# Performance work log

Hardware: AMD Instinct MI355X
Metric: run time of the kernel (lower is better)

The kernel has to match this reference:

```python
import jax, jax.numpy as jnp
import numpy as np
import math

D_MODEL = 1024
HEADS = 16
D_K = D_MODEL // HEADS
BATCH = 4
SEQ = 1024


def setup_inputs() -> dict:
    key = jax.random.key(0)
    ks = jax.random.split(key, 12)
    s = 1.0 / math.sqrt(D_MODEL)
    inp = {
        "q": jax.random.normal(ks[0], (BATCH, SEQ, D_MODEL), jnp.float32),
        "k": jax.random.normal(ks[1], (BATCH, SEQ, D_MODEL), jnp.float32),
        "v": jax.random.normal(ks[2], (BATCH, SEQ, D_MODEL), jnp.float32),
        # causal mask, broadcastable over (batch, heads)
        "mask": jnp.tril(jnp.ones((SEQ, SEQ), jnp.bool_))[None, None, :, :],
        "Wq": jax.random.normal(ks[3], (D_MODEL, D_MODEL), jnp.float32) * s,
        "bq": jax.random.normal(ks[4], (D_MODEL,), jnp.float32) * 0.01,
        "Wk": jax.random.normal(ks[5], (D_MODEL, D_MODEL), jnp.float32) * s,
        "bk": jax.random.normal(ks[6], (D_MODEL,), jnp.float32) * 0.01,
        "Wv": jax.random.normal(ks[7], (D_MODEL, D_MODEL), jnp.float32) * s,
        "bv": jax.random.normal(ks[8], (D_MODEL,), jnp.float32) * 0.01,
        "Wo": jax.random.normal(ks[9], (D_MODEL, D_MODEL), jnp.float32) * s,
        "bo": jax.random.normal(ks[10], (D_MODEL,), jnp.float32) * 0.01,
    }
    return inp


def reference(q, k, v, mask, Wq, bq, Wk, bk, Wv, bv, Wo, bo):
    B, S, _ = q.shape
    # projections (torch Linear: x @ W.T + b; here W stored as [in, out])
    def proj(x, W, b):
        return (x @ W + b).reshape(B, -1, HEADS, D_K).transpose(0, 2, 1, 3)

    Q = proj(q, Wq, bq)  # [B, H, S, Dk]
    K = proj(k, Wk, bk)
    V = proj(v, Wv, bv)

    scores = jnp.einsum("bhqd,bhkd->bhqk", Q, K) / math.sqrt(D_K)
    scores = jnp.where(mask, scores, jnp.float32(-1e9))
    attn = jax.nn.softmax(scores, axis=-1)  # dropout p=0.0 -> identity
    x = jnp.einsum("bhqk,bhkd->bhqd", attn, V)
    x = x.transpose(0, 2, 1, 3).reshape(B, S, D_MODEL)
    return x @ Wo + bo
```

## Files before the change

kernel.cpp:

```cpp
#include <hip/hip_runtime.h>
#include <math.h>

typedef __bf16 bf16_t;
typedef bf16_t bf16x8 __attribute__((ext_vector_type(8)));
typedef bf16_t bf16x4 __attribute__((ext_vector_type(4)));
typedef float  floatx4 __attribute__((ext_vector_type(4)));
typedef unsigned int u32;

#define MFMA_BF16(a, b, c) __builtin_amdgcn_mfma_f32_16x16x32_bf16((a), (b), (c), 0, 0, 0)

#if __has_builtin(__builtin_amdgcn_exp2f)
#define EXP2F(x) __builtin_amdgcn_exp2f(x)
#else
#define EXP2F(x) exp2f(x)
#endif

static constexpr int DMODEL = 1024;
static constexpr int NHEAD  = 16;
static constexpr int HDIM   = 64;
static constexpr int NBATCH = 4;
static constexpr int SEQLEN = 1024;
static constexpr int NTOK   = NBATCH * SEQLEN;

typedef __attribute__((address_space(3))) void       as3_void;
typedef __attribute__((address_space(1))) const void as1_cvoid;

__device__ __forceinline__ void gload16(const void* g, void* l) {
    __builtin_amdgcn_global_load_lds((as1_cvoid*)g, (as3_void*)l, 16, 0, 0);
}

__device__ __forceinline__ bf16x8 load_cvt8(const float* __restrict__ p) {
    floatx4 a = *(const floatx4*)p;
    floatx4 b = *(const floatx4*)(p + 4);
    bf16x8 r;
    r[0] = (bf16_t)a[0]; r[1] = (bf16_t)a[1]; r[2] = (bf16_t)a[2]; r[3] = (bf16_t)a[3];
    r[4] = (bf16_t)b[0]; r[5] = (bf16_t)b[1]; r[6] = (bf16_t)b[2]; r[7] = (bf16_t)b[3];
    return r;
}

__global__ __launch_bounds__(256) void prep(
    const float* __restrict__ W0, const float* __restrict__ W1,
    const float* __restrict__ W2, const float* __restrict__ W3,
    const float* __restrict__ q, const float* __restrict__ k, const float* __restrict__ v,
    bf16_t* __restrict__ Wt, bf16_t* __restrict__ Xr)
{
    __shared__ float tile[32][33];
    const int z = blockIdx.z;
    if (z < 4) {
        const float* W = (z == 0) ? W0 : (z == 1) ? W1 : (z == 2) ? W2 : W3;
        bf16_t* O = Wt + (size_t)z * DMODEL * DMODEL;
        const int tx = threadIdx.x & 31, ty = threadIdx.x >> 5;
        const int r0 = blockIdx.x * 32, c0 = blockIdx.y * 32;
#pragma unroll
        for (int i = 0; i < 32; i += 8)
            tile[ty + i][tx] = W[(size_t)(r0 + ty + i) * DMODEL + c0 + tx];
        __syncthreads();
#pragma unroll
        for (int i = 0; i < 32; i += 8)
            O[(size_t)(c0 + ty + i) * DMODEL + r0 + tx] = (bf16_t)tile[tx][ty + i];
    } else {
        const float* src = (z == 4) ? q : (z == 5) ? k : v;
        bf16_t* dst = Xr + (size_t)(z - 4) * ((size_t)NTOK * DMODEL);
        size_t i = (((size_t)blockIdx.y * 32 + blockIdx.x) * 256 + threadIdx.x) * 16;
        *(bf16x8*)(dst + i)     = load_cvt8(src + i);
        *(bf16x8*)(dst + i + 8) = load_cvt8(src + i + 8);
    }
}

__global__ __launch_bounds__(256) void transpose_w(
    const float* __restrict__ W0, const float* __restrict__ W1,
    const float* __restrict__ W2, const float* __restrict__ W3,
    bf16_t* __restrict__ out)
{
    __shared__ float tile[32][33];
    const float* W = (blockIdx.z == 0) ? W0 : (blockIdx.z == 1) ? W1
                   : (blockIdx.z == 2) ? W2 : W3;
    bf16_t* O = out + (size_t)blockIdx.z * DMODEL * DMODEL;
    int tx = threadIdx.x, ty = threadIdx.y;
    int r0 = blockIdx.x * 32, c0 = blockIdx.y * 32;
#pragma unroll
    for (int i = 0; i < 32; i += 8)
        tile[ty + i][tx] = W[(size_t)(r0 + ty + i) * DMODEL + c0 + tx];
    __syncthreads();
#pragma unroll
    for (int i = 0; i < 32; i += 8)
        O[(size_t)(c0 + ty + i) * DMODEL + r0 + tx] = (bf16_t)tile[tx][ty + i];
}
__global__ __launch_bounds__(256) void cvt_bf16(
    const float* __restrict__ src, bf16_t* __restrict__ dst)
{
    size_t i = ((size_t)blockIdx.x * 256 + threadIdx.x) * 8;
    *(bf16x8*)(dst + i) = load_cvt8(src + i);
}

__global__ __launch_bounds__(256) void gemm_qkv(
    const bf16_t* __restrict__ Xb, size_t astride, int mode0,
    const bf16_t* __restrict__ Wt,
    const float* __restrict__ bq, const float* __restrict__ bk, const float* __restrict__ bv,
    bf16_t* __restrict__ Qh, bf16_t* __restrict__ Kh, bf16_t* __restrict__ Vt)
{
    const int mode = mode0 + blockIdx.z;
    const bf16_t* A = Xb + astride * (size_t)blockIdx.z;
    const bf16_t* B = Wt + (size_t)mode * DMODEL * DMODEL;
    const float* bias = (mode == 0) ? bq : (mode == 1) ? bk : bv;
    bf16_t* out       = (mode == 0) ? Qh : (mode == 1) ? Kh : Vt;

    __shared__ __align__(16) bf16_t lA[2][128 * 32];
    __shared__ __align__(16) bf16_t lB[2][128 * 32];

    const int wave = threadIdx.x >> 6, lane = threadIdx.x & 63;
    const int quad = lane >> 4, l15 = lane & 15;
    const int wm = wave >> 1, wn = wave & 1;
    const int row0 = blockIdx.x * 128, col0 = blockIdx.y * 128;
    const int srow = lane >> 2, scol = (lane & 3) * 8;

    const floatx4 zero = {0.f, 0.f, 0.f, 0.f};
    floatx4 acc[4][4];
#pragma unroll
    for (int mt = 0; mt < 4; mt++)
#pragma unroll
        for (int nt = 0; nt < 4; nt++) acc[mt][nt] = zero;

    const bf16_t* Abase = A + (size_t)(row0 + srow) * DMODEL + scol;
    const bf16_t* Bbase = B + (size_t)(col0 + srow) * DMODEL + scol;

#pragma unroll
    for (int j = 0; j < 2; j++) {
        const int seg = j * 4 + wave;
        gload16(Abase + (size_t)seg * 16 * DMODEL, lA[0] + seg * 512);
        gload16(Bbase + (size_t)seg * 16 * DMODEL, lB[0] + seg * 512);
    }

#pragma unroll
    for (int it = 0; it < 32; it++) {
        __syncthreads();
        const int cur = it & 1;
        if (it + 1 < 32) {
            const int k1 = (it + 1) * 32;
            const int nb = cur ^ 1;
#pragma unroll
            for (int j = 0; j < 2; j++) {
                const int seg = j * 4 + wave;
                gload16(Abase + (size_t)seg * 16 * DMODEL + k1, lA[nb] + seg * 512);
                gload16(Bbase + (size_t)seg * 16 * DMODEL + k1, lB[nb] + seg * 512);
            }
        }
        bf16x8 aF[4], bF[4];
#pragma unroll
        for (int t = 0; t < 4; t++) {
            aF[t] = *(const bf16x8*)(lA[cur] + (wm * 64 + t * 16 + l15) * 32 + quad * 8);
            bF[t] = *(const bf16x8*)(lB[cur] + (wn * 64 + t * 16 + l15) * 32 + quad * 8);
        }
#pragma unroll
        for (int mt = 0; mt < 4; mt++)
#pragma unroll
            for (int nt = 0; nt < 4; nt++)
                acc[mt][nt] = MFMA_BF16(bF[nt], aF[mt], acc[mt][nt]);
    }

    const int hh = (col0 + wn * 64) >> 6;
#pragma unroll
    for (int nt = 0; nt < 4; nt++) {
        const int gn0 = col0 + wn * 64 + nt * 16 + quad * 4;
        const floatx4 bb = *(const floatx4*)&bias[gn0];
        const int dd0 = (wn * 64 + nt * 16 + quad * 4) & 63;
#pragma unroll
        for (int mt = 0; mt < 4; mt++) {
            const int tok = row0 + wm * 64 + mt * 16 + l15;
            const int b = tok >> 10, s = tok & 1023;
            if (mode == 2) {
#pragma unroll
                for (int r = 0; r < 4; r++)
                    Vt[((size_t)((b * NHEAD + hh) * HDIM + dd0 + r)) * SEQLEN + s] =
                        (bf16_t)(acc[mt][nt][r] + bb[r]);
            } else {
                bf16x4 v;
#pragma unroll
                for (int r = 0; r < 4; r++) {
                    float vv = acc[mt][nt][r] + bb[r];
                    if (mode == 0) vv *= 0.1803368801111204f;
                    v[r] = (bf16_t)vv;
                }
                *(bf16x4*)&out[((size_t)((b * NHEAD + hh) * SEQLEN + s)) * HDIM + dd0] = v;
            }
        }
    }
}

__global__ __launch_bounds__(256) void gemm_o(
    const bf16_t* __restrict__ Xa, const bf16_t* __restrict__ Wt,
    const float* __restrict__ bias, float* __restrict__ out)
{
    __shared__ __align__(16) bf16_t lA[2][64 * 32];
    __shared__ __align__(16) bf16_t lB[2][128 * 32];

    const int wave = threadIdx.x >> 6, lane = threadIdx.x & 63;
    const int quad = lane >> 4, l15 = lane & 15;
    const int wm = wave & 1, wn = wave >> 1;
    const int row0 = blockIdx.x * 64, col0 = blockIdx.y * 128;
    const int srow = lane >> 2, scol = (lane & 3) * 8;

    const floatx4 zero = {0.f, 0.f, 0.f, 0.f};
    floatx4 acc[2][4];
#pragma unroll
    for (int mt = 0; mt < 2; mt++)
#pragma unroll
        for (int nt = 0; nt < 4; nt++) acc[mt][nt] = zero;

    const bf16_t* Abase = Xa + (size_t)(row0 + srow) * DMODEL + scol;
    const bf16_t* Bbase = Wt + (size_t)(col0 + srow) * DMODEL + scol;

    gload16(Abase + (size_t)wave * 16 * DMODEL, lA[0] + wave * 512);
#pragma unroll
    for (int j = 0; j < 2; j++) {
        const int seg = wave * 2 + j;
        gload16(Bbase + (size_t)seg * 16 * DMODEL, lB[0] + seg * 512);
    }

#pragma unroll
    for (int it = 0; it < 32; it++) {
        __syncthreads();
        const int cur = it & 1;
        if (it + 1 < 32) {
            const int k1 = (it + 1) * 32;
            const int nb = cur ^ 1;
            gload16(Abase + (size_t)wave * 16 * DMODEL + k1, lA[nb] + wave * 512);
#pragma unroll
            for (int j = 0; j < 2; j++) {
                const int seg = wave * 2 + j;
                gload16(Bbase + (size_t)seg * 16 * DMODEL + k1, lB[nb] + seg * 512);
            }
        }
        bf16x8 aF[2], bF[4];
#pragma unroll
        for (int t = 0; t < 2; t++)
            aF[t] = *(const bf16x8*)(lA[cur] + (wm * 32 + t * 16 + l15) * 32 + quad * 8);
#pragma unroll
        for (int t = 0; t < 4; t++)
            bF[t] = *(const bf16x8*)(lB[cur] + (wn * 64 + t * 16 + l15) * 32 + quad * 8);
#pragma unroll
        for (int mt = 0; mt < 2; mt++)
#pragma unroll
            for (int nt = 0; nt < 4; nt++)
                acc[mt][nt] = MFMA_BF16(bF[nt], aF[mt], acc[mt][nt]);
    }

#pragma unroll
    for (int nt = 0; nt < 4; nt++) {
        const int gn0 = col0 + wn * 64 + nt * 16 + quad * 4;
        const floatx4 bb = *(const floatx4*)&bias[gn0];
#pragma unroll
        for (int mt = 0; mt < 2; mt++) {
            const int tok = row0 + wm * 32 + mt * 16 + l15;
            floatx4 v;
#pragma unroll
            for (int r = 0; r < 4; r++) v[r] = acc[mt][nt][r] + bb[r];
            *(floatx4*)&out[(size_t)tok * DMODEL + gn0] = v;
        }
    }
}

#define SHUF_PV(pk, Vv, oacc) do {                                                     \
    u32 a0 = __shfl(pk.u[0], srcA), a1 = __shfl(pk.u[1], srcA);                        \
    u32 a2 = __shfl(pk.u[0], srcB), a3 = __shfl(pk.u[1], srcB);                        \
    u32 b0 = __shfl(pk.u[2], srcA), b1 = __shfl(pk.u[3], srcA);                        \
    u32 b2 = __shfl(pk.u[2], srcB), b3 = __shfl(pk.u[3], srcB);                        \
    union { u32 u[4]; bf16x8 v; } bP;                                                  \
    bP.u[0] = hiP ? b0 : a0; bP.u[1] = hiP ? b1 : a1;                                  \
    bP.u[2] = hiP ? b2 : a2; bP.u[3] = hiP ? b3 : a3;                                  \
    __builtin_amdgcn_s_setprio(1);                                                     \
    _Pragma("unroll") for (int dt = 0; dt < 4; dt++)                                   \
        oacc[dt] = MFMA_BF16(Vv[dt], bP.v, oacc[dt]);                                  \
    __builtin_amdgcn_s_setprio(0);                                                     \
} while (0)

#define SOFTMAX_PV_FAST(S0x, S1x, Vv, lacc, oacc) do {                                 \
    float ps = 0.f;                                                                    \
    union { bf16_t hh2[8]; u32 u[4]; } pk;                                             \
    _Pragma("unroll") for (int r = 0; r < 4; r++) {                                    \
        float e0 = EXP2F(S0x[r]), e1 = EXP2F(S1x[r]);                                  \
        ps += e0 + e1;                                                                 \
        pk.hh2[r] = (bf16_t)e0; pk.hh2[4 + r] = (bf16_t)e1;                            \
    }                                                                                  \
    lacc += ps;                                                                        \
    SHUF_PV(pk, Vv, oacc);                                                             \
} while (0)

#define SOFTMAX_PV_MASK(S0x, S1x, Vv, kbv, qrow, lacc, oacc) do {                      \
    float ps = 0.f;                                                                    \
    union { bf16_t hh2[8]; u32 u[4]; } pk;                                             \
    _Pragma("unroll") for (int r = 0; r < 4; r++) {                                    \
        const int key0 = (kbv) + quad * 4 + r;                                         \
        float s0 = (key0 <= (qrow))      ? S0x[r] : -1e30f;                            \
        float s1 = (key0 + 16 <= (qrow)) ? S1x[r] : -1e30f;                            \
        float e0 = EXP2F(s0), e1 = EXP2F(s1);                                          \
        ps += e0 + e1;                                                                 \
        pk.hh2[r] = (bf16_t)e0; pk.hh2[4 + r] = (bf16_t)e1;                            \
    }                                                                                  \
    lacc += ps;                                                                        \
    SHUF_PV(pk, Vv, oacc);                                                             \
} while (0)

#define LOAD_KV(K0v, K1v, Vv, kbv) do {                                                \
    _Pragma("unroll") for (int c = 0; c < 2; c++) {                                    \
        K0v[c] = *(const bf16x8*)(Kp + (size_t)((kbv) + l15) * HDIM + c * 32 + quad * 8);      \
        K1v[c] = *(const bf16x8*)(Kp + (size_t)((kbv) + 16 + l15) * HDIM + c * 32 + quad * 8); \
    }                                                                                  \
    _Pragma("unroll") for (int dt = 0; dt < 4; dt++)                                   \
        Vv[dt] = *(const bf16x8*)(Vp + (size_t)(dt * 16 + l15) * SEQLEN + (kbv) + quad * 8);   \
} while (0)

__global__ __launch_bounds__(256, 2) void attn(
    const bf16_t* __restrict__ Qh, const bf16_t* __restrict__ Kh,
    const bf16_t* __restrict__ Vt, bf16_t* __restrict__ X)
{
    __shared__ __align__(8) float comb[2][64][68];
    const int wave = threadIdx.x >> 6, lane = threadIdx.x & 63;
    const int quad = lane >> 4, l15 = lane & 15;
    const int L = blockIdx.x;
    const int bh = (L & 7) * 8 + ((L >> 3) & 7);
    const int j  = L >> 6;
    const int b = bh >> 4, h = bh & 15;

    const int qbase0 = 32 * j,        qbase1 = 32 * j + 16;
    const int qbase2 = 992 - 32 * j,  qbase3 = 1008 - 32 * j;
    const int qrow0 = qbase0 + l15, qrow1 = qbase1 + l15;
    const int qrow2 = qbase2 + l15, qrow3 = qbase3 + l15;
    const int NKA = j + 1, NKB = 32 - j;

    const bf16_t* Qp = Qh + (size_t)bh * SEQLEN * HDIM;
    const bf16_t* Kp = Kh + (size_t)bh * SEQLEN * HDIM;
    const bf16_t* Vp = Vt + (size_t)bh * HDIM * SEQLEN;

    bf16x8 bQ0[2], bQ1[2], bQ2[2], bQ3[2];
#pragma unroll
    for (int c = 0; c < 2; c++) {
        bQ0[c] = *(const bf16x8*)(Qp + (size_t)qrow0 * HDIM + c * 32 + quad * 8);
        bQ1[c] = *(const bf16x8*)(Qp + (size_t)qrow1 * HDIM + c * 32 + quad * 8);
        bQ2[c] = *(const bf16x8*)(Qp + (size_t)qrow2 * HDIM + c * 32 + quad * 8);
        bQ3[c] = *(const bf16x8*)(Qp + (size_t)qrow3 * HDIM + c * 32 + quad * 8);
    }

    const floatx4 zero = {0.f, 0.f, 0.f, 0.f};
    float l0_ = 0.f, l1_ = 0.f, l2_ = 0.f, l3_ = 0.f;
    floatx4 o0[4], o1[4], o2[4], o3[4];
#pragma unroll
    for (int dt = 0; dt < 4; dt++) { o0[dt] = zero; o1[dt] = zero; o2[dt] = zero; o3[dt] = zero; }

    const int srcA = ((quad & 1) ? 32 : 0) + l15;
    const int srcB = srcA + 16;
    const bool hiP = (quad >= 2);

    for (int kc = wave; kc < NKB; kc += 4) {
        const int kb = kc * 32;
        bf16x8 K0[2], K1[2], Vv[4];
        LOAD_KV(K0, K1, Vv, kb);

        const bool doA = (kc < NKA);
        floatx4 S0_0 = zero, S1_0 = zero, S0_1 = zero, S1_1 = zero;
        floatx4 S0_2 = zero, S1_2 = zero, S0_3 = zero, S1_3 = zero;
        __builtin_amdgcn_s_setprio(1);
#pragma unroll
        for (int c = 0; c < 2; c++) {
            S0_2 = MFMA_BF16(K0[c], bQ2[c], S0_2);
            S1_2 = MFMA_BF16(K1[c], bQ2[c], S1_2);
            S0_3 = MFMA_BF16(K0[c], bQ3[c], S0_3);
            S1_3 = MFMA_BF16(K1[c], bQ3[c], S1_3);
        }
        __builtin_amdgcn_s_setprio(0);
        if (doA) {
            __builtin_amdgcn_s_setprio(1);
#pragma unroll
            for (int c = 0; c < 2; c++) {
                S0_0 = MFMA_BF16(K0[c], bQ0[c], S0_0);
                S1_0 = MFMA_BF16(K1[c], bQ0[c], S1_0);
                S0_1 = MFMA_BF16(K0[c], bQ1[c], S0_1);
                S1_1 = MFMA_BF16(K1[c], bQ1[c], S1_1);
            }
            __builtin_amdgcn_s_setprio(0);
        }
        if (kb + 31 <= qbase2) { SOFTMAX_PV_FAST(S0_2, S1_2, Vv, l2_, o2); }
        else                   { SOFTMAX_PV_MASK(S0_2, S1_2, Vv, kb, qrow2, l2_, o2); }
        if (kb + 31 <= qbase3) { SOFTMAX_PV_FAST(S0_3, S1_3, Vv, l3_, o3); }
        else                   { SOFTMAX_PV_MASK(S0_3, S1_3, Vv, kb, qrow3, l3_, o3); }
        if (doA) {
            if (kb + 31 <= qbase0) { SOFTMAX_PV_FAST(S0_0, S1_0, Vv, l0_, o0); }
            else                   { SOFTMAX_PV_MASK(S0_0, S1_0, Vv, kb, qrow0, l0_, o0); }
            if (kb + 31 <= qbase1) { SOFTMAX_PV_FAST(S0_1, S1_1, Vv, l1_, o1); }
            else                   { SOFTMAX_PV_MASK(S0_1, S1_1, Vv, kb, qrow1, l1_, o1); }
        }
    }

    auto publish = [&](int slot) {
        float2* d2 = (float2*)&comb[slot][lane][0];
#pragma unroll
        for (int dt = 0; dt < 4; dt++) {
            d2[ 0 + 2 * dt]     = make_float2(o0[dt][0], o0[dt][1]);
            d2[ 0 + 2 * dt + 1] = make_float2(o0[dt][2], o0[dt][3]);
            d2[ 8 + 2 * dt]     = make_float2(o1[dt][0], o1[dt][1]);
            d2[ 8 + 2 * dt + 1] = make_float2(o1[dt][2], o1[dt][3]);
            d2[16 + 2 * dt]     = make_float2(o2[dt][0], o2[dt][1]);
            d2[16 + 2 * dt + 1] = make_float2(o2[dt][2], o2[dt][3]);
            d2[24 + 2 * dt]     = make_float2(o3[dt][0], o3[dt][1]);
            d2[24 + 2 * dt + 1] = make_float2(o3[dt][2], o3[dt][3]);
        }
        d2[32] = make_float2(l0_, l1_);
        d2[33] = make_float2(l2_, l3_);
    };
    auto accum = [&](int slot) {
        const float2* s2 = (const float2*)&comb[slot][lane][0];
#pragma unroll
        for (int dt = 0; dt < 4; dt++) {
            float2 p0 = s2[ 0 + 2 * dt], p1 = s2[ 0 + 2 * dt + 1];
            float2 q0 = s2[ 8 + 2 * dt], q1 = s2[ 8 + 2 * dt + 1];
            float2 r0 = s2[16 + 2 * dt], r1 = s2[16 + 2 * dt + 1];
            float2 t0 = s2[24 + 2 * dt], t1 = s2[24 + 2 * dt + 1];
            o0[dt][0] += p0.x; o0[dt][1] += p0.y; o0[dt][2] += p1.x; o0[dt][3] += p1.y;
            o1[dt][0] += q0.x; o1[dt][1] += q0.y; o1[dt][2] += q1.x; o1[dt][3] += q1.y;
            o2[dt][0] += r0.x; o2[dt][1] += r0.y; o2[dt][2] += r1.x; o2[dt][3] += r1.y;
            o3[dt][0] += t0.x; o3[dt][1] += t0.y; o3[dt][2] += t1.x; o3[dt][3] += t1.y;
        }
        float2 la = s2[32], lb = s2[33];
        l0_ += la.x; l1_ += la.y; l2_ += lb.x; l3_ += lb.y;
    };

    if (wave & 1) publish(wave >> 1);
    __syncthreads();
    if (!(wave & 1)) accum(wave >> 1);
    __syncthreads();
    if (wave == 2) publish(0);
    __syncthreads();
    if (wave == 0) {
        accum(0);

        l0_ += __shfl_xor(l0_, 16); l0_ += __shfl_xor(l0_, 32);
        l1_ += __shfl_xor(l1_, 16); l1_ += __shfl_xor(l1_, 32);
        l2_ += __shfl_xor(l2_, 16); l2_ += __shfl_xor(l2_, 32);
        l3_ += __shfl_xor(l3_, 16); l3_ += __shfl_xor(l3_, 32);

        const float i0 = 1.f / l0_, i1 = 1.f / l1_, i2 = 1.f / l2_, i3 = 1.f / l3_;
#pragma unroll
        for (int dt = 0; dt < 4; dt++) {
            bf16x4 v0, v1, v2, v3;
#pragma unroll
            for (int r = 0; r < 4; r++) {
                v0[r] = (bf16_t)(o0[dt][r] * i0);
                v1[r] = (bf16_t)(o1[dt][r] * i1);
                v2[r] = (bf16_t)(o2[dt][r] * i2);
                v3[r] = (bf16_t)(o3[dt][r] * i3);
            }
            const size_t cofs = (size_t)h * HDIM + dt * 16 + quad * 4;
            *(bf16x4*)(&X[((size_t)(b * SEQLEN + qrow0)) * DMODEL + cofs]) = v0;
            *(bf16x4*)(&X[((size_t)(b * SEQLEN + qrow1)) * DMODEL + cofs]) = v1;
            *(bf16x4*)(&X[((size_t)(b * SEQLEN + qrow2)) * DMODEL + cofs]) = v2;
            *(bf16x4*)(&X[((size_t)(b * SEQLEN + qrow3)) * DMODEL + cofs]) = v3;
        }
    }
}

extern "C" void kernel_launch(void* const* d_in, const int* in_sizes, int n_in,
                              void* d_out, int out_size, void* d_ws, size_t ws_size,
                              hipStream_t stream)
{
    const float* q  = (const float*)d_in[0];
    const float* k  = (const float*)d_in[1];
    const float* v  = (const float*)d_in[2];
    const float* Wq = (const float*)d_in[4];
    const float* bq = (const float*)d_in[5];
    const float* Wk = (const float*)d_in[6];
    const float* bk = (const float*)d_in[7];
    const float* Wv = (const float*)d_in[8];
    const float* bv = (const float*)d_in[9];
    const float* Wo = (const float*)d_in[10];
    const float* bo = (const float*)d_in[11];
    float* out = (float*)d_out;

    char* ws = (char*)d_ws;
    const size_t MB = 1ull << 20;
    const size_t NELEM = (size_t)NTOK * DMODEL;
    bf16_t* Wt = (bf16_t*)ws;
    bf16_t* Qh = (bf16_t*)(ws + 8 * MB);
    bf16_t* Kh = (bf16_t*)(ws + 16 * MB);
    bf16_t* Vt = (bf16_t*)(ws + 24 * MB);
    bf16_t* Xr = (bf16_t*)(ws + 32 * MB);

    if (ws_size >= 56 * MB) {
        prep<<<dim3(32, 32, 7), dim3(256), 0, stream>>>(Wq, Wk, Wv, Wo, q, k, v, Wt, Xr);
        gemm_qkv<<<dim3(32, 8, 3), dim3(256), 0, stream>>>(
            Xr, NELEM, 0, Wt, bq, bk, bv, Qh, Kh, Vt);
    } else {
        transpose_w<<<dim3(32, 32, 4), dim3(32, 8), 0, stream>>>(Wq, Wk, Wv, Wo, Wt);
        const float* qkv_in[3] = {q, k, v};
        for (int m = 0; m < 3; m++) {
            cvt_bf16<<<dim3(2048), dim3(256), 0, stream>>>(qkv_in[m], Xr);
            gemm_qkv<<<dim3(32, 8, 1), dim3(256), 0, stream>>>(
                Xr, 0, m, Wt, bq, bk, bv, Qh, Kh, Vt);
        }
    }

    bf16_t* Xa = Xr;
    attn<<<dim3(1024), dim3(256), 0, stream>>>(Qh, Kh, Vt, Xa);
    gemm_o<<<dim3(64, 8), dim3(256), 0, stream>>>(
        Xa, Wt + 3 * (size_t)DMODEL * DMODEL, bo, out);
}
```

Measured before the change: 210.4 us.

## Triple-buffer LDS in QKV and output GEMMs with prefetch distance two

Both projection GEMMs move from double to triple LDS buffering. Loads are issued two K-steps ahead, and __syncthreads is replaced by an explicit partial vmcnt wait plus s_barrier, so global-to-LDS loads for the next tiles stay in flight while the current tile is computed. This trades extra shared memory per block, which may lower occupancy, for deeper latency hiding. It also relies on hand-set vmcnt counts matching the number of outstanding loads per wave.

After: 211.7 us. No clear change (+0.6%).

```diff
diff --git a/kernel.cpp b/kernel.cpp
--- a/kernel.cpp
+++ b/kernel.cpp
@@ -105,8 +105,8 @@
     const float* bias = (mode == 0) ? bq : (mode == 1) ? bk : bv;
     bf16_t* out       = (mode == 0) ? Qh : (mode == 1) ? Kh : Vt;
 
-    __shared__ __align__(16) bf16_t lA[2][128 * 32];
-    __shared__ __align__(16) bf16_t lB[2][128 * 32];
+    __shared__ __align__(16) bf16_t lA[3][128 * 32];
+    __shared__ __align__(16) bf16_t lB[3][128 * 32];
 
     const int wave = threadIdx.x >> 6, lane = threadIdx.x & 63;
     const int quad = lane >> 4, l15 = lane & 15;
@@ -125,24 +125,30 @@
     const bf16_t* Bbase = B + (size_t)(col0 + srow) * DMODEL + scol;
 
 #pragma unroll
-    for (int j = 0; j < 2; j++) {
-        const int seg = j * 4 + wave;
-        gload16(Abase + (size_t)seg * 16 * DMODEL, lA[0] + seg * 512);
-        gload16(Bbase + (size_t)seg * 16 * DMODEL, lB[0] + seg * 512);
+    for (int p = 0; p < 2; p++) {
+#pragma unroll
+        for (int j = 0; j < 2; j++) {
+            const int seg = j * 4 + wave;
+            gload16(Abase + (size_t)seg * 16 * DMODEL + p * 32, lA[p] + seg * 512);
+            gload16(Bbase + (size_t)seg * 16 * DMODEL + p * 32, lB[p] + seg * 512);
+        }
     }
 
 #pragma unroll
     for (int it = 0; it < 32; it++) {
-        __syncthreads();
-        const int cur = it & 1;
-        if (it + 1 < 32) {
-            const int k1 = (it + 1) * 32;
-            const int nb = cur ^ 1;
+        if (it < 31) asm volatile("s_waitcnt vmcnt(4)" ::: "memory");
+        else         asm volatile("s_waitcnt vmcnt(0)" ::: "memory");
+        __builtin_amdgcn_s_barrier();
+        __builtin_amdgcn_sched_barrier(0);
+        const int cur = it % 3;
+        if (it + 2 < 32) {
+            const int k2 = (it + 2) * 32;
+            const int nb = (it + 2) % 3;
 #pragma unroll
             for (int j = 0; j < 2; j++) {
                 const int seg = j * 4 + wave;
-                gload16(Abase + (size_t)seg * 16 * DMODEL + k1, lA[nb] + seg * 512);
-                gload16(Bbase + (size_t)seg * 16 * DMODEL + k1, lB[nb] + seg * 512);
+                gload16(Abase + (size_t)seg * 16 * DMODEL + k2, lA[nb] + seg * 512);
+                gload16(Bbase + (size_t)seg * 16 * DMODEL + k2, lB[nb] + seg * 512);
             }
         }
         bf16x8 aF[4], bF[4];
@@ -191,8 +197,8 @@
     const bf16_t* __restrict__ Xa, const bf16_t* __restrict__ Wt,
     const float* __restrict__ bias, float* __restrict__ out)
 {
-    __shared__ __align__(16) bf16_t lA[2][64 * 32];
-    __shared__ __align__(16) bf16_t lB[2][128 * 32];
+    __shared__ __align__(16) bf16_t lA[3][64 * 32];
+    __shared__ __align__(16) bf16_t lB[3][128 * 32];
 
     const int wave = threadIdx.x >> 6, lane = threadIdx.x & 63;
     const int quad = lane >> 4, l15 = lane & 15;
@@ -210,25 +216,31 @@
     const bf16_t* Abase = Xa + (size_t)(row0 + srow) * DMODEL + scol;
     const bf16_t* Bbase = Wt + (size_t)(col0 + srow) * DMODEL + scol;
 
-    gload16(Abase + (size_t)wave * 16 * DMODEL, lA[0] + wave * 512);
-#pragma unroll
-    for (int j = 0; j < 2; j++) {
-        const int seg = wave * 2 + j;
-        gload16(Bbase + (size_t)seg * 16 * DMODEL, lB[0] + seg * 512);
+#pragma unroll
+    for (int p = 0; p < 2; p++) {
+        gload16(Abase + (size_t)wave * 16 * DMODEL + p * 32, lA[p] + wave * 512);
+#pragma unroll
+        for (int j = 0; j < 2; j++) {
+            const int seg = wave * 2 + j;
+            gload16(Bbase + (size_t)seg * 16 * DMODEL + p * 32, lB[p] + seg * 512);
+        }
     }
 
 #pragma unroll
     for (int it = 0; it < 32; it++) {
-        __syncthreads();
-        const int cur = it & 1;
-        if (it + 1 < 32) {
-            const int k1 = (it + 1) * 32;
-            const int nb = cur ^ 1;
-            gload16(Abase + (size_t)wave * 16 * DMODEL + k1, lA[nb] + wave * 512);
+        if (it < 31) asm volatile("s_waitcnt vmcnt(3)" ::: "memory");
+        else         asm volatile("s_waitcnt vmcnt(0)" ::: "memory");
+        __builtin_amdgcn_s_barrier();
+        __builtin_amdgcn_sched_barrier(0);
+        const int cur = it % 3;
+        if (it + 2 < 32) {
+            const int k2 = (it + 2) * 32;
+            const int nb = (it + 2) % 3;
+            gload16(Abase + (size_t)wave * 16 * DMODEL + k2, lA[nb] + wave * 512);
 #pragma unroll
             for (int j = 0; j < 2; j++) {
                 const int seg = wave * 2 + j;
-                gload16(Bbase + (size_t)seg * 16 * DMODEL + k1, lB[nb] + seg * 512);
+                gload16(Bbase + (size_t)seg * 16 * DMODEL + k2, lB[nb] + seg * 512);
             }
         }
         bf16x8 aF[2], bF[4];
```
